# Kernel optimization log

Hardware: AMD Instinct MI355X
Metric: run time of the kernel (lower is better)

The kernel has to match this reference:

```python
import jax, jax.numpy as jnp
import numpy as np

N = 100000      # total nodes
E = 800000      # directed edges
DIN = 256       # input feature dim
H = 128         # hidden dim
EPS = 1e-5      # BatchNorm eps


def setup_inputs() -> dict:
    key = jax.random.key(0)
    ks = jax.random.split(key, 18)
    s = 0.05
    return {
        "x": jax.random.normal(ks[0], (N, DIN), jnp.float32),
        "src": jax.random.randint(ks[1], (E,), 0, N, dtype=jnp.int32),
        "dst": jax.random.randint(ks[2], (E,), 0, N, dtype=jnp.int32),
        "W1": jax.random.normal(ks[3], (DIN, H), jnp.float32) * s,
        "b1": jnp.zeros((H,), jnp.float32),
        "g1": jnp.ones((H,), jnp.float32),
        "be1": jnp.zeros((H,), jnp.float32),
        "W2": jax.random.normal(ks[4], (H, H), jnp.float32) * s,
        "b2": jnp.zeros((H,), jnp.float32),
        "g2": jnp.ones((H,), jnp.float32),
        "be2": jnp.zeros((H,), jnp.float32),
        "W3": jax.random.normal(ks[5], (H, H), jnp.float32) * s,
        "b3": jnp.zeros((H,), jnp.float32),
        "g3": jnp.ones((H,), jnp.float32),
        "be3": jnp.zeros((H,), jnp.float32),
        "Wf": jax.random.normal(ks[6], (H, 1), jnp.float32) * s,
        "bf": jnp.zeros((1,), jnp.float32),
    }


def _gcn_conv(h, W, b, src, dst, dis):
    # GCNConv: project, then sym-normalized aggregation over edges + self-loops
    h = h @ W                                   # [N, out]
    coef = dis[src] * dis[dst]                  # [E] edge norm weights
    agg = jax.ops.segment_sum(h[src] * coef[:, None], dst, num_segments=N)
    agg = agg + h * (dis * dis)[:, None]        # self-loop term (norm = 1/deg)
    return agg + b


def _bn_relu(h, g, be):
    # BatchNorm1d in training mode (batch stats over nodes, biased variance)
    mu = jnp.mean(h, axis=0)
    var = jnp.var(h, axis=0)
    return jax.nn.relu((h - mu) * (g / jnp.sqrt(var + EPS)) + be)


def reference(x, src, dst, W1, b1, g1, be1, W2, b2, g2, be2,
              W3, b3, g3, be3, Wf, bf):
    # degree of (A + I) counted on destination nodes, edge weight 1
    deg = jax.ops.segment_sum(jnp.ones((E,), jnp.float32), dst, num_segments=N) + 1.0
    dis = jax.lax.rsqrt(deg)                    # deg >= 1, safe

    h = _bn_relu(_gcn_conv(x, W1, b1, src, dst, dis), g1, be1)
    h = _bn_relu(_gcn_conv(h, W2, b2, src, dst, dis), g2, be2)
    h = _bn_relu(_gcn_conv(h, W3, b3, src, dst, dis), g3, be3)
    return h @ Wf + bf                          # [N, 1]
```

## Files before the change

kernel.cpp:

```cpp
#include <hip/hip_runtime.h>
#include <hip/hip_bf16.h>

typedef unsigned short ushort_t;
typedef __bf16 bf16x8 __attribute__((ext_vector_type(8)));
typedef unsigned short ushort8 __attribute__((ext_vector_type(8)));
typedef unsigned short ushort4v __attribute__((ext_vector_type(4)));
typedef float f32x4 __attribute__((ext_vector_type(4)));

#define HH 128
#define EPS 1e-5f
#define STAT_SLICES 32
#define GAS __attribute__((address_space(1)))
#define LAS __attribute__((address_space(3)))

__device__ __forceinline__ float bf2f(ushort_t u) {
    unsigned v = ((unsigned)u) << 16;
    return __builtin_bit_cast(float, v);
}
__device__ __forceinline__ ushort_t f2bf(float f) {
    unsigned u = __builtin_bit_cast(unsigned, f);
    unsigned r = (u + 0x7fffu + ((u >> 16) & 1u)) >> 16;
    return (ushort_t)r;
}
__device__ __forceinline__ float cvt(const void* p, int i, int flag) {
    return flag ? bf2f(((const ushort_t*)p)[i]) : ((const float*)p)[i];
}
__device__ __forceinline__ void dma16(const void* g, void* l) {
    __builtin_amdgcn_global_load_lds((const GAS unsigned*)g, (LAS unsigned*)l, 16, 0, 0);
}
__device__ __forceinline__ void acc8(const uint4 w, float c, float a[8]) {
    unsigned x0 = w.x, x1 = w.y, x2 = w.z, x3 = w.w;
    a[0] = fmaf(__builtin_bit_cast(float, x0 << 16), c, a[0]);
    a[1] = fmaf(__builtin_bit_cast(float, x0 & 0xffff0000u), c, a[1]);
    a[2] = fmaf(__builtin_bit_cast(float, x1 << 16), c, a[2]);
    a[3] = fmaf(__builtin_bit_cast(float, x1 & 0xffff0000u), c, a[3]);
    a[4] = fmaf(__builtin_bit_cast(float, x2 << 16), c, a[4]);
    a[5] = fmaf(__builtin_bit_cast(float, x2 & 0xffff0000u), c, a[5]);
    a[6] = fmaf(__builtin_bit_cast(float, x3 << 16), c, a[6]);
    a[7] = fmaf(__builtin_bit_cast(float, x3 & 0xffff0000u), c, a[7]);
}

__global__ void preK(const int* __restrict__ dst, int* __restrict__ counts, int E,
                     const void* W1, ushort_t* Wt1, const void* W2, ushort_t* Wt2,
                     const void* W3, ushort_t* Wt3,
                     const void* g1, const void* b1, const void* b2, const void* b3,
                     const void* g2, const void* g3, const void* be1, const void* be2,
                     const void* be3, const void* Wfp, const void* bfp,
                     float* __restrict__ cvec, int histB) {
    const int bid = blockIdx.x;
    const int tid = threadIdx.x;
    const int flag = (((const ushort_t*)g1)[0] == 0x3F80) ? 1 : 0;
    if (bid < histB) {
        int e = bid * 256 + tid;
        if (e < E) atomicAdd(&counts[dst[e]], 1);
    } else if (bid < histB + 256) {
        int idx = (bid - histB) * 256 + tid;
        const void* W; ushort_t* Wt; int K;
        if (idx < 32768)      { W = W1; Wt = Wt1; K = 256; }
        else if (idx < 49152) { W = W2; Wt = Wt2; K = 128; idx -= 32768; }
        else                  { W = W3; Wt = Wt3; K = 128; idx -= 49152; }
        int k = idx >> 7, nn = idx & 127;
        Wt[nn * K + k] = flag ? ((const ushort_t*)W)[idx] : f2bf(((const float*)W)[idx]);
    } else {
        int t = tid;
        if (t < 128) {
            cvec[t]        = cvt(b1, t, flag);
            cvec[128 + t]  = cvt(b2, t, flag);
            cvec[256 + t]  = cvt(b3, t, flag);
            cvec[384 + t]  = cvt(g1, t, flag);
            cvec[512 + t]  = cvt(g2, t, flag);
            cvec[640 + t]  = cvt(g3, t, flag);
            cvec[768 + t]  = cvt(be1, t, flag);
            cvec[896 + t]  = cvt(be2, t, flag);
            cvec[1024 + t] = cvt(be3, t, flag);
            cvec[1152 + t] = cvt(Wfp, t, flag);
            if (t == 0) cvec[1280] = cvt(bfp, 0, flag);
        }
    }
}

__global__ void scanAdisK(const int* __restrict__ cnt, int* __restrict__ partial,
                          float* __restrict__ dis, int n, int nbScan) {
    __shared__ int lds[256];
    const int tid = threadIdx.x;
    if ((int)blockIdx.x < nbScan) {
        int base = blockIdx.x * 2048 + tid * 8;
        int s = 0;
#pragma unroll
        for (int j = 0; j < 8; ++j) { int idx = base + j; if (idx < n) s += cnt[idx]; }
        lds[tid] = s; __syncthreads();
        for (int off = 128; off; off >>= 1) { if (tid < off) lds[tid] += lds[tid + off]; __syncthreads(); }
        if (tid == 0) partial[blockIdx.x] = lds[0];
    } else {
        int i = (blockIdx.x - nbScan) * 256 + tid;
        if (i < n) dis[i] = rsqrtf((float)cnt[i] + 1.0f);
    }
}

__device__ __forceinline__ void scanC2Dev(int* lds, const int* __restrict__ cnt,
                                          const int* __restrict__ partial,
                                          int* __restrict__ rowptr, int n, int bid, int nb) {
    const int tid = threadIdx.x;
    int pre = 0, tot = 0;
    for (int i = 0; i < nb; ++i) { int v = partial[i]; if (i < bid) pre += v; tot += v; }
    int base = bid * 2048 + tid * 8;
    int v[8]; int s = 0;
#pragma unroll
    for (int j = 0; j < 8; ++j) { int idx = base + j; v[j] = (idx < n) ? cnt[idx] : 0; s += v[j]; }
    lds[tid] = s; __syncthreads();
    for (int off = 1; off < 256; off <<= 1) {
        int x = (tid >= off) ? lds[tid - off] : 0;
        __syncthreads();
        lds[tid] += x;
        __syncthreads();
    }
    int excl = lds[tid] - s;
    int off0 = pre + excl;
#pragma unroll
    for (int j = 0; j < 8; ++j) {
        int idx = base + j;
        if (idx < n) { rowptr[idx] = off0; off0 += v[j]; }
    }
    if (bid == 0 && tid == 0) rowptr[n] = tot;
}

__global__ void scatterK(const int* __restrict__ src, const int* __restrict__ dst,
                         const int* __restrict__ rowptr, int* __restrict__ fill,
                         const float* __restrict__ dis,
                         uint2* __restrict__ erec, int E) {
    int e = blockIdx.x * 256 + threadIdx.x;
    if (e >= E) return;
    int d = dst[e], s = src[e];
    int old = atomicSub(&fill[d], 1);
    int pos = rowptr[d] + old - 1;
    float c = dis[s] * dis[d];
    uint2 r; r.x = (unsigned)s; r.y = __builtin_bit_cast(unsigned, c);
    erec[pos] = r;
}

__global__ __launch_bounds__(256) void mm1scanCK(const void* __restrict__ x,
                                                 const ushort_t* __restrict__ Wt1,
                                                 ushort_t* __restrict__ tbuf, int n,
                                                 const ushort_t* __restrict__ flagRef,
                                                 const int* __restrict__ cnt,
                                                 const int* __restrict__ partial,
                                                 int* __restrict__ rowptr, int nbScan) {
    __shared__ char smem[65536];
    const int tid = threadIdx.x;
    if ((int)blockIdx.x < nbScan) {
        scanC2Dev((int*)smem, cnt, partial, rowptr, n, blockIdx.x - 0, nbScan);
        return;
    }
    const int arm = blockIdx.x - nbScan;
    const int ch  = arm & 1;

#pragma unroll
    for (int it = 0; it < 8; ++it) {
        int idx = tid + it * 256;
        int r = idx >> 5, seg = idx & 31;
        int p = seg ^ (r & 7);
        *(uint4*)&smem[r * 512 + p * 16] = *(const uint4*)&Wt1[(size_t)(ch * 64 + r) * 256 + seg * 8];
    }
    __syncthreads();

    const int lane = tid & 63, wave = tid >> 6;
    const int m = lane & 15, q = lane >> 4;
    const int flag = (flagRef[0] == 0x3F80) ? 1 : 0;
    const int nTiles = (n + 63) >> 6;
    char* abuf = smem + 32768;

    for (int tile = (arm >> 1); tile < nTiles; tile += 256) {
        const int row0 = tile * 64 + wave * 16;
        if (flag) {
#pragma unroll
            for (int j = 0; j < 8; ++j) {
                int r = row0 + j * 2;
                if (r + 1 >= n) r = n - 2;
                const char* g = (const char*)x + (size_t)r * 512 + lane * 16;
                dma16(g, abuf + (wave * 16 + j * 2) * 512);
            }
            __builtin_amdgcn_s_waitcnt(0x0F70);
        } else {
#pragma unroll
            for (int j = 0; j < 8; ++j) {
                int r = row0 + j * 2;
                if (r + 1 >= n) r = n - 2;
                int rr = r + (lane >> 5);
                int off = (lane & 31) * 8;
                const float* p = (const float*)x + (size_t)rr * 256 + off;
                float4 f0 = *(const float4*)p, f1 = *(const float4*)(p + 4);
                ushort8 v;
                v[0] = f2bf(f0.x); v[1] = f2bf(f0.y); v[2] = f2bf(f0.z); v[3] = f2bf(f0.w);
                v[4] = f2bf(f1.x); v[5] = f2bf(f1.y); v[6] = f2bf(f1.z); v[7] = f2bf(f1.w);
                *(ushort8*)&abuf[(wave * 16 + j * 2) * 512 + lane * 16] = v;
            }
        }

        f32x4 acc[4];
#pragma unroll
        for (int t = 0; t < 4; ++t) acc[t] = (f32x4){0.f, 0.f, 0.f, 0.f};
        const char* arow = abuf + (wave * 16 + m) * 512;
#pragma unroll
        for (int s = 0; s < 8; ++s) {
            ushort8 av = *(const ushort8*)(arow + s * 64 + q * 16);
            bf16x8 nf = __builtin_bit_cast(bf16x8, av);
#pragma unroll
            for (int t = 0; t < 4; ++t) {
                int p = (s * 4 + q) ^ (m & 7);
                ushort8 wv = *(const ushort8*)&smem[(t * 16 + m) * 512 + p * 16];
                acc[t] = __builtin_amdgcn_mfma_f32_16x16x32_bf16(
                    __builtin_bit_cast(bf16x8, wv), nf, acc[t], 0, 0, 0);
            }
        }
        int node = tile * 64 + wave * 16 + m;
        if (node < n) {
            ushort_t* op = tbuf + (size_t)node * HH + ch * 64 + q * 4;
#pragma unroll
            for (int t = 0; t < 4; ++t) {
                ushort4v pk;
#pragma unroll
                for (int r = 0; r < 4; ++r) pk[r] = f2bf(acc[t][r]);
                *(ushort4v*)(op + t * 16) = pk;
            }
        }
    }
}

__global__ __launch_bounds__(256) void mmBNK(const ushort_t* __restrict__ A,
                                             const ushort_t* __restrict__ Wt,
                                             ushort_t* __restrict__ out, int n,
                                             const float* __restrict__ ssum,
                                             const float* __restrict__ ssq,
                                             const float* __restrict__ gam,
                                             const float* __restrict__ bet) {
    __shared__ char smem[50176];
    char* abuf = smem + 32768;
    float* scw = (float*)(smem + 49152);
    const int tid = threadIdx.x;

    if (tid < 128) {
        float S = 0.f, Q = 0.f;
#pragma unroll
        for (int sl = 0; sl < STAT_SLICES; ++sl) { S += ssum[sl * HH + tid]; Q += ssq[sl * HH + tid]; }
        float invn = 1.0f / (float)n;
        float mu = S * invn;
        float var = fmaxf(Q * invn - mu * mu, 0.f);
        float sc = gam[tid] * rsqrtf(var + EPS);
        scw[tid] = sc;
        scw[128 + tid] = bet[tid] - mu * sc;
    }
#pragma unroll
    for (int it = 0; it < 8; ++it) {
        int idx = tid + it * 256;
        int r = idx >> 4, seg = idx & 15;
        int p = seg ^ (r & 7);
        *(uint4*)&smem[r * 256 + p * 16] = *(const uint4*)&Wt[(size_t)r * 128 + seg * 8];
    }
    __syncthreads();

    const int lane = tid & 63, wave = tid >> 6;
    const int m = lane & 15, q = lane >> 4;
    const int nTiles = (n + 63) >> 6;

    for (int tile = blockIdx.x; tile < nTiles; tile += gridDim.x) {
        const int row0 = tile * 64 + wave * 16;
#pragma unroll
        for (int j = 0; j < 4; ++j) {
            int r = row0 + j * 4;
            if (r + 3 >= n) r = n - 4;
            const char* g = (const char*)A + (size_t)r * 256 + lane * 16;
            dma16(g, abuf + (wave * 16 + j * 4) * 256);
        }
        __builtin_amdgcn_s_waitcnt(0x0F70);

        f32x4 acc[8];
#pragma unroll
        for (int t = 0; t < 8; ++t) acc[t] = (f32x4){0.f, 0.f, 0.f, 0.f};
        const char* arow = abuf + (wave * 16 + m) * 256;
#pragma unroll
        for (int s = 0; s < 4; ++s) {
            ushort8 av = *(const ushort8*)(arow + s * 64 + q * 16);
            int kb = s * 32 + q * 8;
#pragma unroll
            for (int j = 0; j < 8; ++j)
                av[j] = f2bf(fmaxf(bf2f(av[j]) * scw[kb + j] + scw[128 + kb + j], 0.f));
            bf16x8 nf = __builtin_bit_cast(bf16x8, av);
#pragma unroll
            for (int t = 0; t < 8; ++t) {
                int p = (s * 4 + q) ^ (m & 7);
                ushort8 wv = *(const ushort8*)&smem[(t * 16 + m) * 256 + p * 16];
                acc[t] = __builtin_amdgcn_mfma_f32_16x16x32_bf16(
                    __builtin_bit_cast(bf16x8, wv), nf, acc[t], 0, 0, 0);
            }
        }
        int node = tile * 64 + wave * 16 + m;
        if (node < n) {
            ushort_t* op = out + (size_t)node * HH + q * 4;
#pragma unroll
            for (int t = 0; t < 8; ++t) {
                ushort4v pk;
#pragma unroll
                for (int r = 0; r < 4; ++r) pk[r] = f2bf(acc[t][r]);
                *(ushort4v*)(op + t * 16) = pk;
            }
        }
    }
}

__global__ __launch_bounds__(256) void aggK(const ushort_t* __restrict__ t,
                                            const uint2* __restrict__ erec,
                                            const int* __restrict__ rowptr,
                                            const float* __restrict__ dis,
                                            const float* __restrict__ bias,
                                            ushort_t* __restrict__ g,
                                            float* __restrict__ ssum, float* __restrict__ ssq,
                                            int n) {
    const int tid  = threadIdx.x;
    const int lane = tid & 63;
    const int wave = tid >> 6;
    const int grp  = lane >> 4;
    const int p    = lane & 15;
    const int cb   = p * 8;

    float bch[8];
#pragma unroll
    for (int j = 0; j < 8; ++j) bch[j] = bias[cb + j];

    float s[8], q[8];
#pragma unroll
    for (int j = 0; j < 8; ++j) { s[j] = 0.f; q[j] = 0.f; }

    for (int node = blockIdx.x * 16 + wave * 4 + grp; node < n; node += gridDim.x * 16) {
        float d = dis[node];
        float d2 = d * d;
        float a[8];
#pragma unroll
        for (int j = 0; j < 8; ++j) a[j] = 0.f;
        uint4 sv = *(const uint4*)(t + (size_t)node * HH + cb);
        acc8(sv, d2, a);

        int beg = rowptr[node], end = rowptr[node + 1];
        for (int eb = beg; eb < end; eb += 16) {
            int rem = end - eb; if (rem > 16) rem = 16;
            uint2 rec = (p < rem) ? erec[eb + p] : (uint2){0u, 0u};
            int es = (int)rec.x;
            float ec = __builtin_bit_cast(float, rec.y);
            int rr = (rem + 3) & ~3;
            for (int k = 0; k < rr; k += 4) {
                uint4 ww[4]; float c2[4];
#pragma unroll
                for (int kk = 0; kk < 4; ++kk) {
                    int sl = (lane & 48) + k + kk;
                    int ii = __shfl(es, sl);
                    float cv = __shfl(ec, sl);
                    c2[kk] = (k + kk < rem) ? cv : 0.f;
                    ww[kk] = *(const uint4*)(t + (size_t)ii * HH + cb);
                }
#pragma unroll
                for (int kk = 0; kk < 4; ++kk) acc8(ww[kk], c2[kk], a);
            }
        }
        ushort8 pk;
#pragma unroll
        for (int j = 0; j < 8; ++j) {
            a[j] += bch[j];
            pk[j] = f2bf(a[j]);
            s[j] += a[j]; q[j] += a[j] * a[j];
        }
        *(ushort8*)(g + (size_t)node * HH + cb) = pk;
    }

#pragma unroll
    for (int j = 0; j < 8; ++j) {
        s[j] += __shfl_xor(s[j], 16); s[j] += __shfl_xor(s[j], 32);
        q[j] += __shfl_xor(q[j], 16); q[j] += __shfl_xor(q[j], 32);
    }
    __shared__ float red[4][16][16];
    if (grp == 0) {
#pragma unroll
        for (int j = 0; j < 8; ++j) { red[wave][p][j] = s[j]; red[wave][p][8 + j] = q[j]; }
    }
    __syncthreads();
    {
        int ch = tid & 127, kind = tid >> 7;
        float S = 0.f;
#pragma unroll
        for (int w = 0; w < 4; ++w) S += red[w][ch >> 3][kind * 8 + (ch & 7)];
        int slice = (blockIdx.x & (STAT_SLICES - 1)) * HH;
        atomicAdd((kind ? ssq : ssum) + slice + ch, S);
    }
}

__global__ __launch_bounds__(256) void outK(const ushort_t* __restrict__ g,
                                            const float* __restrict__ ssum,
                                            const float* __restrict__ ssq,
                                            const float* __restrict__ gam,
                                            const float* __restrict__ bet,
                                            const float* __restrict__ Wf,
                                            const float* __restrict__ bfp,
                                            void* __restrict__ outv, int n,
                                            const ushort_t* __restrict__ flagRef) {
    __shared__ float scw[256];
    const int tid = threadIdx.x;
    if (tid < 128) {
        float S = 0.f, Q = 0.f;
#pragma unroll
        for (int sl = 0; sl < STAT_SLICES; ++sl) { S += ssum[sl * HH + tid]; Q += ssq[sl * HH + tid]; }
        float invn = 1.0f / (float)n;
        float mu = S * invn;
        float var = fmaxf(Q * invn - mu * mu, 0.f);
        float sc = gam[tid] * rsqrtf(var + EPS);
        scw[tid] = sc;
        scw[128 + tid] = bet[tid] - mu * sc;
    }
    __syncthreads();

    const int lane = tid & 63;
    const int wave = tid >> 6;
    const int grp  = lane >> 4;
    const int p    = lane & 15;
    const int cb   = p * 8;
    float w8[8], sc8[8], sh8[8];
#pragma unroll
    for (int j = 0; j < 8; ++j) {
        w8[j] = Wf[cb + j]; sc8[j] = scw[cb + j]; sh8[j] = scw[128 + cb + j];
    }
    const float bb = bfp[0];
    const int flag = (flagRef[0] == 0x3F80) ? 1 : 0;

    for (int node = blockIdx.x * 16 + wave * 4 + grp; node < n; node += gridDim.x * 16) {
        uint4 v = *(const uint4*)(g + (size_t)node * HH + cb);
        unsigned u[4] = {v.x, v.y, v.z, v.w};
        float x = 0.f;
#pragma unroll
        for (int j = 0; j < 4; ++j) {
            float f0 = __builtin_bit_cast(float, u[j] << 16);
            float f1 = __builtin_bit_cast(float, u[j] & 0xffff0000u);
            x += fmaxf(f0 * sc8[2 * j] + sh8[2 * j], 0.f) * w8[2 * j];
            x += fmaxf(f1 * sc8[2 * j + 1] + sh8[2 * j + 1], 0.f) * w8[2 * j + 1];
        }
#pragma unroll
        for (int off = 8; off; off >>= 1) x += __shfl_xor(x, off);
        if (p == 0) {
            float r = x + bb;
            if (flag) ((ushort_t*)outv)[node] = f2bf(r);
            else      ((float*)outv)[node] = r;
        }
    }
}

extern "C" void kernel_launch(void* const* d_in, const int* in_sizes, int n_in,
                              void* d_out, int out_size, void* d_ws, size_t ws_size,
                              hipStream_t stream) {
    const int DIN = 256;
    const int N = in_sizes[0] / DIN;
    const int E = in_sizes[1];

    const void* x   = d_in[0];
    const int*  src = (const int*)d_in[1];
    const int*  dst = (const int*)d_in[2];
    const void* W1  = d_in[3];
    const void* b1  = d_in[4];
    const void* g1  = d_in[5];
    const void* be1 = d_in[6];
    const void* W2  = d_in[7];
    const void* b2  = d_in[8];
    const void* g2  = d_in[9];
    const void* be2 = d_in[10];
    const void* W3  = d_in[11];
    const void* b3  = d_in[12];
    const void* g3  = d_in[13];
    const void* be3 = d_in[14];
    const void* Wf  = d_in[15];
    const void* bfp = d_in[16];
    const ushort_t* flagRef = (const ushort_t*)g1;

    char* base = (char*)d_ws;
    size_t off = 0;
    auto carve = [&](size_t bytes) -> void* {
        void* p = base + off;
        off += (bytes + 255) & ~(size_t)255;
        return p;
    };
    int*      counts = (int*)carve((size_t)N * 4);
    float*    stats  = (float*)carve((size_t)3 * 2 * STAT_SLICES * HH * 4);
    size_t    zbytes = off;
    float*    dis    = (float*)carve((size_t)N * 4);
    int*      rowptr = (int*)carve((size_t)(N + 1) * 4);
    int*      partial= (int*)carve(256 * 4);
    uint2*    erec   = (uint2*)carve((size_t)E * 8);
    ushort_t* Wt1    = (ushort_t*)carve((size_t)128 * 256 * 2);
    ushort_t* Wt2    = (ushort_t*)carve((size_t)128 * 128 * 2);
    ushort_t* Wt3    = (ushort_t*)carve((size_t)128 * 128 * 2);
    ushort_t* tbuf   = (ushort_t*)carve((size_t)N * HH * 2);
    ushort_t* gbuf   = (ushort_t*)carve((size_t)N * HH * 2);
    float*    cvec   = (float*)carve((size_t)1281 * 4);

    float* ssum0 = stats;                         float* ssq0 = ssum0 + STAT_SLICES * HH;
    float* ssum1 = ssq0 + STAT_SLICES * HH;       float* ssq1 = ssum1 + STAT_SLICES * HH;
    float* ssum2 = ssq1 + STAT_SLICES * HH;       float* ssq2 = ssum2 + STAT_SLICES * HH;

    float* c_b1 = cvec;         float* c_b2 = cvec + 128;  float* c_b3 = cvec + 256;
    float* c_g1 = cvec + 384;   float* c_g2 = cvec + 512;  float* c_g3 = cvec + 640;
    float* c_be1 = cvec + 768;  float* c_be2 = cvec + 896; float* c_be3 = cvec + 1024;
    float* c_Wf = cvec + 1152;  float* c_bf = cvec + 1280;

    const int nbScan = (N + 2047) / 2048;
    const int histB  = (E + 255) / 256;
    const int disB   = (N + 255) / 256;
    const int aggB   = 2048;

    hipMemsetAsync(d_ws, 0, zbytes, stream);

    preK<<<histB + 256 + 1, 256, 0, stream>>>(dst, counts, E, W1, Wt1, W2, Wt2, W3, Wt3,
                                              g1, b1, b2, b3, g2, g3, be1, be2, be3, Wf, bfp,
                                              cvec, histB);
    scanAdisK<<<nbScan + disB, 256, 0, stream>>>(counts, partial, dis, N, nbScan);
    mm1scanCK<<<nbScan + 512, 256, 0, stream>>>(x, Wt1, tbuf, N, flagRef,
                                                counts, partial, rowptr, nbScan);
    scatterK<<<histB, 256, 0, stream>>>(src, dst, rowptr, counts, dis, erec, E);

    aggK<<<aggB, 256, 0, stream>>>(tbuf, erec, rowptr, dis, c_b1, gbuf, ssum0, ssq0, N);
    mmBNK<<<768, 256, 0, stream>>>(gbuf, Wt2, tbuf, N, ssum0, ssq0, c_g1, c_be1);
    aggK<<<aggB, 256, 0, stream>>>(tbuf, erec, rowptr, dis, c_b2, gbuf, ssum1, ssq1, N);
    mmBNK<<<768, 256, 0, stream>>>(gbuf, Wt3, tbuf, N, ssum1, ssq1, c_g2, c_be2);
    aggK<<<aggB, 256, 0, stream>>>(tbuf, erec, rowptr, dis, c_b3, gbuf, ssum2, ssq2, N);
    outK<<<1024, 256, 0, stream>>>(gbuf, ssum2, ssq2, c_g3, c_be3, c_Wf, c_bf, d_out, N, flagRef);
}
```

Baseline: 419.3 us.

## Compute full 128-column output per block with register-prefetched A tiles

Each block of the first projection GEMM now loads the whole 128x256 weight matrix into shared memory and produces all 128 output columns, where before each block produced half. This stops the input rows being read twice. The A operand is no longer staged through LDS with DMA. Each lane loads its fragments straight into registers, and the next tile is prefetched into a second register set while the current tile's MFMAs run. The cost is higher register pressure (8 accumulators plus two 8-vector fragment sets), which may lower occupancy. Per-lane A loads are strided rather than fully coalesced rows.

```diff
diff --git a/kernel.cpp b/kernel.cpp
--- a/kernel.cpp
+++ b/kernel.cpp
@@ -148,18 +148,17 @@
     __shared__ char smem[65536];
     const int tid = threadIdx.x;
     if ((int)blockIdx.x < nbScan) {
-        scanC2Dev((int*)smem, cnt, partial, rowptr, n, blockIdx.x - 0, nbScan);
+        scanC2Dev((int*)smem, cnt, partial, rowptr, n, blockIdx.x, nbScan);
         return;
     }
     const int arm = blockIdx.x - nbScan;
-    const int ch  = arm & 1;
-
-#pragma unroll
-    for (int it = 0; it < 8; ++it) {
+
+#pragma unroll
+    for (int it = 0; it < 16; ++it) {
         int idx = tid + it * 256;
         int r = idx >> 5, seg = idx & 31;
         int p = seg ^ (r & 7);
-        *(uint4*)&smem[r * 512 + p * 16] = *(const uint4*)&Wt1[(size_t)(ch * 64 + r) * 256 + seg * 8];
+        *(uint4*)&smem[r * 512 + p * 16] = *(const uint4*)&Wt1[(size_t)r * 256 + seg * 8];
     }
     __syncthreads();
 
@@ -167,46 +166,45 @@
     const int m = lane & 15, q = lane >> 4;
     const int flag = (flagRef[0] == 0x3F80) ? 1 : 0;
     const int nTiles = (n + 63) >> 6;
-    char* abuf = smem + 32768;
-
-    for (int tile = (arm >> 1); tile < nTiles; tile += 256) {
-        const int row0 = tile * 64 + wave * 16;
+
+    auto loadA = [&](int tile, ushort8 af[8]) {
+        int node = tile * 64 + wave * 16 + m;
+        int rr = node < n ? node : n - 1;
         if (flag) {
-#pragma unroll
-            for (int j = 0; j < 8; ++j) {
-                int r = row0 + j * 2;
-                if (r + 1 >= n) r = n - 2;
-                const char* g = (const char*)x + (size_t)r * 512 + lane * 16;
-                dma16(g, abuf + (wave * 16 + j * 2) * 512);
-            }
-            __builtin_amdgcn_s_waitcnt(0x0F70);
+            const ushort_t* ap = (const ushort_t*)x + (size_t)rr * 256 + q * 8;
+#pragma unroll
+            for (int s = 0; s < 8; ++s) af[s] = *(const ushort8*)(ap + s * 32);
         } else {
-#pragma unroll
-            for (int j = 0; j < 8; ++j) {
-                int r = row0 + j * 2;
-                if (r + 1 >= n) r = n - 2;
-                int rr = r + (lane >> 5);
-                int off = (lane & 31) * 8;
-                const float* p = (const float*)x + (size_t)rr * 256 + off;
-                float4 f0 = *(const float4*)p, f1 = *(const float4*)(p + 4);
+            const float* ap = (const float*)x + (size_t)rr * 256 + q * 8;
+#pragma unroll
+            for (int s = 0; s < 8; ++s) {
+                float4 f0 = *(const float4*)(ap + s * 32);
+                float4 f1 = *(const float4*)(ap + s * 32 + 4);
                 ushort8 v;
                 v[0] = f2bf(f0.x); v[1] = f2bf(f0.y); v[2] = f2bf(f0.z); v[3] = f2bf(f0.w);
                 v[4] = f2bf(f1.x); v[5] = f2bf(f1.y); v[6] = f2bf(f1.z); v[7] = f2bf(f1.w);
-                *(ushort8*)&abuf[(wave * 16 + j * 2) * 512 + lane * 16] = v;
+                af[s] = v;
             }
         }
-
-        f32x4 acc[4];
-#pragma unroll
-        for (int t = 0; t < 4; ++t) acc[t] = (f32x4){0.f, 0.f, 0.f, 0.f};
-        const char* arow = abuf + (wave * 16 + m) * 512;
+    };
+
+    ushort8 afA[8];
+    if (arm < nTiles) loadA(arm, afA);
+
+    for (int tile = arm; tile < nTiles; tile += 512) {
+        ushort8 afB[8];
+        int nx = tile + 512;
+        if (nx < nTiles) loadA(nx, afB);
+
+        f32x4 acc[8];
+#pragma unroll
+        for (int t = 0; t < 8; ++t) acc[t] = (f32x4){0.f, 0.f, 0.f, 0.f};
 #pragma unroll
         for (int s = 0; s < 8; ++s) {
-            ushort8 av = *(const ushort8*)(arow + s * 64 + q * 16);
-            bf16x8 nf = __builtin_bit_cast(bf16x8, av);
-#pragma unroll
-            for (int t = 0; t < 4; ++t) {
-                int p = (s * 4 + q) ^ (m & 7);
+            bf16x8 nf = __builtin_bit_cast(bf16x8, afA[s]);
+            int p = (s * 4 + q) ^ (m & 7);
+#pragma unroll
+            for (int t = 0; t < 8; ++t) {
                 ushort8 wv = *(const ushort8*)&smem[(t * 16 + m) * 512 + p * 16];
                 acc[t] = __builtin_amdgcn_mfma_f32_16x16x32_bf16(
                     __builtin_bit_cast(bf16x8, wv), nf, acc[t], 0, 0, 0);
@@ -214,15 +212,17 @@
         }
         int node = tile * 64 + wave * 16 + m;
         if (node < n) {
-            ushort_t* op = tbuf + (size_t)node * HH + ch * 64 + q * 4;
-#pragma unroll
-            for (int t = 0; t < 4; ++t) {
+            ushort_t* op = tbuf + (size_t)node * HH + q * 4;
+#pragma unroll
+            for (int t = 0; t < 8; ++t) {
                 ushort4v pk;
 #pragma unroll
                 for (int r = 0; r < 4; ++r) pk[r] = f2bf(acc[t][r]);
                 *(ushort4v*)(op + t * 16) = pk;
             }
         }
+#pragma unroll
+        for (int s = 0; s < 8; ++s) afA[s] = afB[s];
     }
 }
 
```

Result: slower. 428.9 us (+2.3%).
